# Kernel tuning notes

Hardware: AMD Instinct MI355X
Metric: run time of the kernel (lower is better)

The kernel has to match this reference:

```python
import jax, jax.numpy as jnp
import numpy as np
from jax import lax

NUM_VARS = 64
T_MAX = 2048
EMBED_DIM = 512
GRU_H = 64
FINAL_H = 64
OUT_DIM = 1


def setup_inputs() -> dict:
    key = jax.random.key(0)
    ks = jax.random.split(key, 12)
    s_e = 1.0 / np.sqrt(EMBED_DIM)
    s_h = 1.0 / np.sqrt(GRU_H)
    s_c = 1.0 / np.sqrt(NUM_VARS * GRU_H)
    s_f = 1.0 / np.sqrt(FINAL_H)
    return {
        "embeddings": jax.random.normal(ks[0], (NUM_VARS, T_MAX, EMBED_DIM), jnp.float32),
        "lengths": jax.random.randint(ks[1], (NUM_VARS,), 0, T_MAX),
        # GRU params, PyTorch layout: gate order r, z, n
        "W_ih": jax.random.uniform(ks[2], (3 * GRU_H, EMBED_DIM), jnp.float32, -s_h, s_h),
        "W_hh": jax.random.uniform(ks[3], (3 * GRU_H, GRU_H), jnp.float32, -s_h, s_h),
        "b_ih": jax.random.uniform(ks[4], (3 * GRU_H,), jnp.float32, -s_h, s_h),
        "b_hh": jax.random.uniform(ks[5], (3 * GRU_H,), jnp.float32, -s_h, s_h),
        # MLP params
        "W1": jax.random.uniform(ks[6], (FINAL_H, NUM_VARS * GRU_H), jnp.float32, -s_c, s_c),
        "b1": jax.random.uniform(ks[7], (FINAL_H,), jnp.float32, -s_c, s_c),
        "W2": jax.random.uniform(ks[8], (OUT_DIM, FINAL_H), jnp.float32, -s_f, s_f),
        "b2": jax.random.uniform(ks[9], (OUT_DIM,), jnp.float32, -s_f, s_f),
    }


def _gru_final_hidden(embeddings, lengths, W_ih, W_hh, b_ih, b_hh):
    # embeddings: [V, T, E]; shared GRU run over all variables in one batched scan.
    V, T, E = embeddings.shape
    H = W_hh.shape[1]
    # Precompute input-to-gate projections for all timesteps: [V, T, 3H] -> [T, V, 3H]
    x_gates = jnp.einsum('vte,ge->tvg', embeddings, W_ih) + b_ih

    def step(h, inp):
        xg, t = inp  # xg: [V, 3H]
        hg = h @ W_hh.T + b_hh  # [V, 3H]
        xr, xz, xn = jnp.split(xg, 3, axis=-1)
        hr, hz, hn = jnp.split(hg, 3, axis=-1)
        r = jax.nn.sigmoid(xr + hr)
        z = jax.nn.sigmoid(xz + hz)
        n = jnp.tanh(xn + r * hn)
        h_new = (1.0 - z) * n + z * h
        # freeze state past each variable's length (length 0 -> stays zeros)
        h = jnp.where((t < lengths)[:, None], h_new, h)
        return h, None

    h0 = jnp.zeros((V, H), embeddings.dtype)
    hT, _ = lax.scan(step, h0, (x_gates, jnp.arange(T)))
    return hT  # [V, H]


def reference(embeddings, lengths, W_ih, W_hh, b_ih, b_hh, W1, b1, W2, b2):
    hT = _gru_final_hidden(embeddings, lengths, W_ih, W_hh, b_ih, b_hh)
    concat = hT.reshape(-1)  # [V*H], same order as torch.cat of per-var summaries
    hid = jax.nn.relu(concat @ W1.T + b1)
    return hid @ W2.T + b2  # [out_dim]
```

## Files before the change

### kernel.cpp

```cpp
#include <hip/hip_runtime.h>
#include <math.h>

#define V 64
#define TMAX 2048
#define ED 512
#define H 64
#define G3 192

__global__ void k_init(float* __restrict__ h) {
    int i = blockIdx.x * blockDim.x + threadIdx.x;
    if (i < V * H) h[i] = 0.f;
}

__global__ __launch_bounds__(256) void k_gemm(
    const float* __restrict__ emb, const int* __restrict__ lengths,
    const float* __restrict__ W_ih, const float* __restrict__ b_ih,
    float* __restrict__ xg, int c, int CT) {
    int v   = blockIdx.y;
    int tl0 = blockIdx.x * 128;
    int t0  = c * CT + tl0;
    int len = lengths[v];
    if (t0 >= len) return;

    __shared__ __align__(16) float Es[128 * 64];
    __shared__ __align__(16) float Ws[G3 * 64];

    int th = threadIdx.x;
    int tb = th & 15;
    int gb = th >> 4;
    int eswz = tb & 7;

    float acc[8][12];
#pragma unroll
    for (int i = 0; i < 8; i++)
#pragma unroll
        for (int j = 0; j < 12; j++) acc[i][j] = 0.f;

    const float* ebase = emb + (size_t)(v * TMAX + t0) * ED;

    for (int kc = 0; kc < 8; kc++) {
#pragma unroll
        for (int r = 0; r < 8; r++) {
            int i = th + r * 256;
            int row = i >> 4, pos = i & 15;
            *(float4*)&Es[row * 64 + (pos ^ ((row >> 3) & 7)) * 4] =
                *(const float4*)&ebase[(size_t)row * ED + kc * 64 + pos * 4];
        }
#pragma unroll
        for (int r = 0; r < 12; r++) {
            int i = th + r * 256;
            int row = i >> 4, pos = i & 15;
            *(float4*)&Ws[row * 64 + (pos ^ (row & 7)) * 4] =
                *(const float4*)&W_ih[(size_t)row * ED + kc * 64 + pos * 4];
        }
        __syncthreads();
#pragma unroll 2
        for (int k4 = 0; k4 < 16; k4++) {
            float4 e[8];
#pragma unroll
            for (int i = 0; i < 8; i++)
                e[i] = *(float4*)&Es[(tb * 8 + i) * 64 + (k4 ^ eswz) * 4];
#pragma unroll
            for (int j = 0; j < 12; j++) {
                int g = gb * 12 + j;
                float4 w = *(float4*)&Ws[g * 64 + (k4 ^ (g & 7)) * 4];
#pragma unroll
                for (int i = 0; i < 8; i++)
                    acc[i][j] += e[i].x * w.x + e[i].y * w.y + e[i].z * w.z + e[i].w * w.w;
            }
        }
        __syncthreads();
    }

    float4 bv[3];
#pragma unroll
    for (int j4 = 0; j4 < 3; j4++)
        bv[j4] = *(const float4*)&b_ih[gb * 12 + j4 * 4];

#pragma unroll
    for (int i = 0; i < 8; i++) {
        size_t ob = ((size_t)(v * CT + tl0 + tb * 8 + i)) * G3 + gb * 12;
#pragma unroll
        for (int j4 = 0; j4 < 3; j4++) {
            float4 o;
            o.x = acc[i][j4 * 4 + 0] + bv[j4].x;
            o.y = acc[i][j4 * 4 + 1] + bv[j4].y;
            o.z = acc[i][j4 * 4 + 2] + bv[j4].z;
            o.w = acc[i][j4 * 4 + 3] + bv[j4].w;
            *(float4*)&xg[ob + j4 * 4] = o;
        }
    }
}

__global__ __launch_bounds__(256) void k_gemm_s(
    const float* __restrict__ emb, const int* __restrict__ lengths,
    const float* __restrict__ W_ih, const float* __restrict__ b_ih,
    float* __restrict__ xg, int c, int CT) {
    int v   = blockIdx.y;
    int tl0 = blockIdx.x * 32;
    int t0  = c * CT + tl0;
    int len = lengths[v];
    if (t0 >= len) return;

    __shared__ __align__(16) float Es[32][68];
    __shared__ __align__(16) float Ws[G3][68];

    int th = threadIdx.x;
    int tq = th & 31;
    int gq = th >> 5;

    float acc[24];
#pragma unroll
    for (int j = 0; j < 24; j++) acc[j] = 0.f;

    for (int kc = 0; kc < 8; kc++) {
#pragma unroll
        for (int r = 0; r < 2; r++) {
            int i = th + r * 256;
            int row = i >> 4, pos = i & 15;
            *(float4*)&Es[row][pos * 4] =
                *(const float4*)&emb[((size_t)(v * TMAX + t0 + row)) * ED + kc * 64 + pos * 4];
        }
#pragma unroll
        for (int r = 0; r < 12; r++) {
            int i = th + r * 256;
            int row = i >> 4, pos = i & 15;
            *(float4*)&Ws[row][pos * 4] =
                *(const float4*)&W_ih[(size_t)row * ED + kc * 64 + pos * 4];
        }
        __syncthreads();
#pragma unroll
        for (int k4 = 0; k4 < 16; k4++) {
            float4 e4 = *(float4*)&Es[tq][k4 * 4];
#pragma unroll
            for (int j = 0; j < 24; j++) {
                float4 w4 = *(float4*)&Ws[gq * 24 + j][k4 * 4];
                acc[j] += e4.x * w4.x + e4.y * w4.y + e4.z * w4.z + e4.w * w4.w;
            }
        }
        __syncthreads();
    }

    size_t ob = ((size_t)(v * CT + tl0 + tq)) * G3 + gq * 24;
#pragma unroll
    for (int j4 = 0; j4 < 6; j4++) {
        float4 o;
        o.x = acc[j4 * 4 + 0] + b_ih[gq * 24 + j4 * 4 + 0];
        o.y = acc[j4 * 4 + 1] + b_ih[gq * 24 + j4 * 4 + 1];
        o.z = acc[j4 * 4 + 2] + b_ih[gq * 24 + j4 * 4 + 2];
        o.w = acc[j4 * 4 + 3] + b_ih[gq * 24 + j4 * 4 + 3];
        *(float4*)&xg[ob + j4 * 4] = o;
    }
}

__global__ __launch_bounds__(192) void k_rec(
    const float* __restrict__ xg, const int* __restrict__ lengths,
    const float* __restrict__ W_hh, const float* __restrict__ b_hh,
    float* __restrict__ h, int c, int CT) {
    int v  = blockIdx.x;
    int th = threadIdx.x;
    int len = lengths[v];
    int rem = len - c * CT;
    int tcnt = rem < 0 ? 0 : (rem > CT ? CT : rem);

    __shared__ __align__(16) float hs[H];
    __shared__ float znbuf[128];

    float4 w4[16];
#pragma unroll
    for (int k4 = 0; k4 < 16; k4++)
        w4[k4] = *(const float4*)&W_hh[(size_t)th * H + k4 * 4];
    float bhh = b_hh[th];

    if (th < H) hs[th] = h[v * H + th];
    __syncthreads();

    const float* xgv = xg + (size_t)v * CT * G3;
    float xr = 0.f, xz = 0.f, xn = 0.f;
    if (th < H && tcnt > 0) {
        xr = xgv[th]; xz = xgv[64 + th]; xn = xgv[128 + th];
    }

    for (int t = 0; t < tcnt; t++) {
        float pr = 0.f, pz = 0.f, pn = 0.f;
        if (th < H && t + 1 < tcnt) {
            const float* p = xgv + (size_t)(t + 1) * G3;
            pr = p[th]; pz = p[64 + th]; pn = p[128 + th];
        }
        float a0 = 0.f, a1 = 0.f, a2 = 0.f, a3 = 0.f;
#pragma unroll
        for (int k4 = 0; k4 < 4; k4++) {
            float4 h4 = *(float4*)&hs[k4 * 4];
            a0 += w4[k4].x * h4.x + w4[k4].y * h4.y + w4[k4].z * h4.z + w4[k4].w * h4.w;
        }
#pragma unroll
        for (int k4 = 4; k4 < 8; k4++) {
            float4 h4 = *(float4*)&hs[k4 * 4];
            a1 += w4[k4].x * h4.x + w4[k4].y * h4.y + w4[k4].z * h4.z + w4[k4].w * h4.w;
        }
#pragma unroll
        for (int k4 = 8; k4 < 12; k4++) {
            float4 h4 = *(float4*)&hs[k4 * 4];
            a2 += w4[k4].x * h4.x + w4[k4].y * h4.y + w4[k4].z * h4.z + w4[k4].w * h4.w;
        }
#pragma unroll
        for (int k4 = 12; k4 < 16; k4++) {
            float4 h4 = *(float4*)&hs[k4 * 4];
            a3 += w4[k4].x * h4.x + w4[k4].y * h4.y + w4[k4].z * h4.z + w4[k4].w * h4.w;
        }
        float hg = bhh + ((a0 + a1) + (a2 + a3));

        if (th >= H) znbuf[th - H] = hg;
        __syncthreads();
        if (th < H) {
            float r = __fdividef(1.f, 1.f + __expf(-(hg + xr)));
            float z = __fdividef(1.f, 1.f + __expf(-(znbuf[th] + xz)));
            float pre = xn + r * znbuf[64 + th];
            float e2 = __expf(2.f * pre);
            float n = 1.f - __fdividef(2.f, e2 + 1.f);
            float hold = hs[th];
            hs[th] = (1.f - z) * n + z * hold;
            xr = pr; xz = pz; xn = pn;
        }
        __syncthreads();
    }
    if (th < H) h[v * H + th] = hs[th];
}

__global__ __launch_bounds__(192) void k_rec_fused(
    const float* __restrict__ emb, const int* __restrict__ lengths,
    const float* __restrict__ W_ih, const float* __restrict__ b_ih,
    const float* __restrict__ W_hh, const float* __restrict__ b_hh,
    float* __restrict__ h) {
    int v  = blockIdx.x;
    int th = threadIdx.x;
    int len = lengths[v];

    __shared__ __align__(16) float hs[H];
    __shared__ __align__(16) float es[ED];
    __shared__ float znbuf[128];
    __shared__ float xnbuf[64];

    float4 w4[16];
#pragma unroll
    for (int k4 = 0; k4 < 16; k4++)
        w4[k4] = *(const float4*)&W_hh[(size_t)th * H + k4 * 4];
    float bhh = b_hh[th];
    float bih = b_ih[th];
    if (th < H) hs[th] = 0.f;
    const float* ev = emb + (size_t)v * TMAX * ED;
    const float* wrow = W_ih + (size_t)th * ED;

    for (int t = 0; t < len; t++) {
        __syncthreads();
        for (int i = th; i < 128; i += 192)
            *(float4*)&es[i * 4] = *(const float4*)&ev[(size_t)t * ED + i * 4];
        __syncthreads();
        float xgt = bih;
        for (int k4 = 0; k4 < 128; k4++) {
            float4 wv = *(const float4*)&wrow[k4 * 4];
            float4 e4 = *(float4*)&es[k4 * 4];
            xgt += wv.x * e4.x + wv.y * e4.y + wv.z * e4.z + wv.w * e4.w;
        }
        float hg = bhh;
#pragma unroll
        for (int k4 = 0; k4 < 16; k4++) {
            float4 h4 = *(float4*)&hs[k4 * 4];
            hg += w4[k4].x * h4.x + w4[k4].y * h4.y + w4[k4].z * h4.z + w4[k4].w * h4.w;
        }
        if (th >= H && th < 128) znbuf[th - H] = hg + xgt;
        if (th >= 128) { znbuf[th - H] = hg; xnbuf[th - 128] = xgt; }
        __syncthreads();
        if (th < H) {
            float r = 1.f / (1.f + expf(-(hg + xgt)));
            float z = 1.f / (1.f + expf(-znbuf[th]));
            float n = tanhf(xnbuf[th] + r * znbuf[64 + th]);
            float hold = hs[th];
            hs[th] = (1.f - z) * n + z * hold;
        }
    }
    __syncthreads();
    if (th < H) h[v * H + th] = hs[th];
}

__global__ __launch_bounds__(256) void k_mlp1(
    const float* __restrict__ h, const float* __restrict__ W1,
    const float* __restrict__ b1, float* __restrict__ hid) {
    int o = blockIdx.x, th = threadIdx.x;
    const float* w = W1 + (size_t)o * (V * H);
    float s = 0.f;
#pragma unroll
    for (int r = 0; r < 4; r++) {
        int i = (th + r * 256) * 4;
        float4 a = *(const float4*)&w[i];
        float4 b = *(const float4*)&h[i];
        s += a.x * b.x + a.y * b.y + a.z * b.z + a.w * b.w;
    }
    __shared__ float red[4];
    for (int off = 32; off; off >>= 1) s += __shfl_down(s, off);
    if ((th & 63) == 0) red[th >> 6] = s;
    __syncthreads();
    if (th == 0) {
        float tot = red[0] + red[1] + red[2] + red[3] + b1[o];
        hid[o] = tot > 0.f ? tot : 0.f;
    }
}

__global__ void k_mlp2(const float* __restrict__ hid, const float* __restrict__ W2,
                       const float* __restrict__ b2, float* __restrict__ out) {
    int th = threadIdx.x;
    float s = hid[th] * W2[th];
    for (int off = 32; off; off >>= 1) s += __shfl_down(s, off);
    if (th == 0) out[0] = s + b2[0];
}

extern "C" void kernel_launch(void* const* d_in, const int* in_sizes, int n_in,
                              void* d_out, int out_size, void* d_ws, size_t ws_size,
                              hipStream_t stream) {
    const float* emb     = (const float*)d_in[0];
    const int*   lengths = (const int*)d_in[1];
    const float* W_ih    = (const float*)d_in[2];
    const float* W_hh    = (const float*)d_in[3];
    const float* b_ih    = (const float*)d_in[4];
    const float* b_hh    = (const float*)d_in[5];
    const float* W1      = (const float*)d_in[6];
    const float* b1      = (const float*)d_in[7];
    const float* W2      = (const float*)d_in[8];
    const float* b2      = (const float*)d_in[9];
    float* out = (float*)d_out;
    float* wsf = (float*)d_ws;

    const size_t tail = (size_t)V * H + V;
    int CT = 0;
    const int cts[7] = {2048, 1024, 512, 256, 128, 64, 32};
    for (int i = 0; i < 7; i++) {
        size_t need = ((size_t)V * cts[i] * G3 + tail) * sizeof(float);
        if (need <= ws_size) { CT = cts[i]; break; }
    }

    if (CT > 0) {
        float* xg  = wsf;
        float* hbf = wsf + (size_t)V * CT * G3;
        float* hid = hbf + (size_t)V * H;
        k_init<<<dim3((V * H + 255) / 256), dim3(256), 0, stream>>>(hbf);
        int nch = TMAX / CT;
        for (int c = 0; c < nch; c++) {
            if (CT >= 256)
                k_gemm<<<dim3(CT / 128, V), dim3(256), 0, stream>>>(emb, lengths, W_ih, b_ih, xg, c, CT);
            else
                k_gemm_s<<<dim3(CT / 32, V), dim3(256), 0, stream>>>(emb, lengths, W_ih, b_ih, xg, c, CT);
            k_rec<<<dim3(V), dim3(G3), 0, stream>>>(xg, lengths, W_hh, b_hh, hbf, c, CT);
        }
        k_mlp1<<<dim3(V), dim3(256), 0, stream>>>(hbf, W1, b1, hid);
        k_mlp2<<<dim3(1), dim3(64), 0, stream>>>(hid, W2, b2, out);
    } else {
        float* hbf = wsf;
        float* hid = hbf + (size_t)V * H;
        k_rec_fused<<<dim3(V), dim3(G3), 0, stream>>>(emb, lengths, W_ih, b_ih, W_hh, b_hh, hbf);
        k_mlp1<<<dim3(V), dim3(256), 0, stream>>>(hbf, W1, b1, hid);
        k_mlp2<<<dim3(1), dim3(64), 0, stream>>>(hid, W2, b2, out);
    }
}
```

Baseline: 1.841 ms.

## Run GRU recurrence with one wavefront per variable using packed FMA

Restructures the recurrent kernel from 192 threads (one per gate row) to 64 threads, where each thread holds all three gate rows of W_hh in registers and computes r, z and n itself. This removes the shared-memory exchange buffer and both __syncthreads per timestep, relying on single-wavefront lockstep to keep the hidden-state shared array consistent. The dot products use v_pk_fma_f32 inline assembly to do two FMAs per instruction. It raises register use to about 192 floats of weights per thread and depends on wave64 execution with no barrier between the write and the next read of the shared state.

```diff
diff --git a/kernel.cpp b/kernel.cpp
--- a/kernel.cpp
+++ b/kernel.cpp
@@ -6,6 +6,10 @@
 #define ED 512
 #define H 64
 #define G3 192
+
+__device__ __forceinline__ void pk_fma(float2& acc, float2 a, float2 b) {
+    asm("v_pk_fma_f32 %0, %1, %2, %0" : "+v"(acc) : "v"(a), "v"(b));
+}
 
 __global__ void k_init(float* __restrict__ h) {
     int i = blockIdx.x * blockDim.x + threadIdx.x;
@@ -153,78 +157,71 @@
     }
 }
 
-__global__ __launch_bounds__(192) void k_rec(
+__global__ __launch_bounds__(64) void k_rec(
     const float* __restrict__ xg, const int* __restrict__ lengths,
     const float* __restrict__ W_hh, const float* __restrict__ b_hh,
     float* __restrict__ h, int c, int CT) {
-    int v  = blockIdx.x;
-    int th = threadIdx.x;
+    int v = blockIdx.x;
+    int i = threadIdx.x;
     int len = lengths[v];
     int rem = len - c * CT;
     int tcnt = rem < 0 ? 0 : (rem > CT ? CT : rem);
 
     __shared__ __align__(16) float hs[H];
-    __shared__ float znbuf[128];
-
-    float4 w4[16];
-#pragma unroll
-    for (int k4 = 0; k4 < 16; k4++)
-        w4[k4] = *(const float4*)&W_hh[(size_t)th * H + k4 * 4];
-    float bhh = b_hh[th];
-
-    if (th < H) hs[th] = h[v * H + th];
-    __syncthreads();
+
+    float2 wr[32], wz[32], wn[32];
+    {
+        const float2* Wr = (const float2*)&W_hh[(size_t)i * H];
+        const float2* Wz = (const float2*)&W_hh[(size_t)(64 + i) * H];
+        const float2* Wn = (const float2*)&W_hh[(size_t)(128 + i) * H];
+#pragma unroll
+        for (int k = 0; k < 32; k++) { wr[k] = Wr[k]; wz[k] = Wz[k]; wn[k] = Wn[k]; }
+    }
+    float br = b_hh[i], bz = b_hh[64 + i], bn = b_hh[128 + i];
+
+    float hown = h[v * H + i];
+    hs[i] = hown;
 
     const float* xgv = xg + (size_t)v * CT * G3;
     float xr = 0.f, xz = 0.f, xn = 0.f;
-    if (th < H && tcnt > 0) {
-        xr = xgv[th]; xz = xgv[64 + th]; xn = xgv[128 + th];
-    }
+    if (tcnt > 0) { xr = xgv[i]; xz = xgv[64 + i]; xn = xgv[128 + i]; }
 
     for (int t = 0; t < tcnt; t++) {
         float pr = 0.f, pz = 0.f, pn = 0.f;
-        if (th < H && t + 1 < tcnt) {
+        if (t + 1 < tcnt) {
             const float* p = xgv + (size_t)(t + 1) * G3;
-            pr = p[th]; pz = p[64 + th]; pn = p[128 + th];
-        }
-        float a0 = 0.f, a1 = 0.f, a2 = 0.f, a3 = 0.f;
-#pragma unroll
-        for (int k4 = 0; k4 < 4; k4++) {
-            float4 h4 = *(float4*)&hs[k4 * 4];
-            a0 += w4[k4].x * h4.x + w4[k4].y * h4.y + w4[k4].z * h4.z + w4[k4].w * h4.w;
-        }
-#pragma unroll
-        for (int k4 = 4; k4 < 8; k4++) {
-            float4 h4 = *(float4*)&hs[k4 * 4];
-            a1 += w4[k4].x * h4.x + w4[k4].y * h4.y + w4[k4].z * h4.z + w4[k4].w * h4.w;
-        }
-#pragma unroll
-        for (int k4 = 8; k4 < 12; k4++) {
-            float4 h4 = *(float4*)&hs[k4 * 4];
-            a2 += w4[k4].x * h4.x + w4[k4].y * h4.y + w4[k4].z * h4.z + w4[k4].w * h4.w;
-        }
-#pragma unroll
-        for (int k4 = 12; k4 < 16; k4++) {
-            float4 h4 = *(float4*)&hs[k4 * 4];
-            a3 += w4[k4].x * h4.x + w4[k4].y * h4.y + w4[k4].z * h4.z + w4[k4].w * h4.w;
-        }
-        float hg = bhh + ((a0 + a1) + (a2 + a3));
-
-        if (th >= H) znbuf[th - H] = hg;
-        __syncthreads();
-        if (th < H) {
-            float r = __fdividef(1.f, 1.f + __expf(-(hg + xr)));
-            float z = __fdividef(1.f, 1.f + __expf(-(znbuf[th] + xz)));
-            float pre = xn + r * znbuf[64 + th];
-            float e2 = __expf(2.f * pre);
-            float n = 1.f - __fdividef(2.f, e2 + 1.f);
-            float hold = hs[th];
-            hs[th] = (1.f - z) * n + z * hold;
-            xr = pr; xz = pz; xn = pn;
-        }
-        __syncthreads();
-    }
-    if (th < H) h[v * H + th] = hs[th];
+            pr = p[i]; pz = p[64 + i]; pn = p[128 + i];
+        }
+        float2 ar0 = {0.f,0.f}, ar1 = {0.f,0.f};
+        float2 az0 = {0.f,0.f}, az1 = {0.f,0.f};
+        float2 an0 = {0.f,0.f}, an1 = {0.f,0.f};
+#pragma unroll
+        for (int q = 0; q < 16; q++) {
+            float4 h4 = *(const float4*)&hs[q * 4];
+            float2 hlo = make_float2(h4.x, h4.y);
+            float2 hhi = make_float2(h4.z, h4.w);
+            pk_fma(ar0, wr[2 * q],     hlo);
+            pk_fma(ar1, wr[2 * q + 1], hhi);
+            pk_fma(az0, wz[2 * q],     hlo);
+            pk_fma(az1, wz[2 * q + 1], hhi);
+            pk_fma(an0, wn[2 * q],     hlo);
+            pk_fma(an1, wn[2 * q + 1], hhi);
+        }
+        float hr = br + ((ar0.x + ar0.y) + (ar1.x + ar1.y));
+        float hz = bz + ((az0.x + az0.y) + (az1.x + az1.y));
+        float hn = bn + ((an0.x + an0.y) + (an1.x + an1.y));
+
+        float r = __fdividef(1.f, 1.f + __expf(-(hr + xr)));
+        float z = __fdividef(1.f, 1.f + __expf(-(hz + xz)));
+        float pre = xn + r * hn;
+        float e2 = __expf(2.f * pre);
+        float n = 1.f - __fdividef(2.f, e2 + 1.f);
+        hown = (1.f - z) * n + z * hown;
+
+        hs[i] = hown;
+        xr = pr; xz = pz; xn = pn;
+    }
+    if (tcnt > 0) h[v * H + i] = hown;
 }
 
 __global__ __launch_bounds__(192) void k_rec_fused(
@@ -349,7 +346,7 @@
                 k_gemm<<<dim3(CT / 128, V), dim3(256), 0, stream>>>(emb, lengths, W_ih, b_ih, xg, c, CT);
             else
                 k_gemm_s<<<dim3(CT / 32, V), dim3(256), 0, stream>>>(emb, lengths, W_ih, b_ih, xg, c, CT);
-            k_rec<<<dim3(V), dim3(G3), 0, stream>>>(xg, lengths, W_hh, b_hh, hbf, c, CT);
+            k_rec<<<dim3(V), dim3(64), 0, stream>>>(xg, lengths, W_hh, b_hh, hbf, c, CT);
         }
         k_mlp1<<<dim3(V), dim3(256), 0, stream>>>(hbf, W1, b1, hid);
         k_mlp2<<<dim3(1), dim3(64), 0, stream>>>(hid, W2, b2, out);
```

After: 2.165 ms. 1.18x slower.

## Restructure GRU recurrence to split gate nonlinearities across warps with packed FMA

Applied to the files above, without the earlier changes.

The recurrent kernel now has each of the three 64-thread groups compute its own gate activation: the r and z groups apply sigmoid and publish it to shared memory, and the n group finishes the update. This replaces the previous scheme where one group did all the nonlinear work serially. The inner dot products use v_pk_fma_f32 packed FMAs, and the loop is unrolled by four timesteps with xg prefetched a group ahead (indices clamped and masked by tcnt). Waves-per-EU attributes are also set on both kernels. The change aims to shorten the per-step serial critical path, at the cost of inline asm and a fixed occupancy hint.

```diff
diff --git a/kernel.cpp b/kernel.cpp
--- a/kernel.cpp
+++ b/kernel.cpp
@@ -7,12 +7,17 @@
 #define H 64
 #define G3 192
 
+__device__ __forceinline__ void pk_fma(float2& acc, float2 a, float2 b) {
+    asm("v_pk_fma_f32 %0, %1, %2, %0" : "+v"(acc) : "v"(a), "v"(b));
+}
+
 __global__ void k_init(float* __restrict__ h) {
     int i = blockIdx.x * blockDim.x + threadIdx.x;
     if (i < V * H) h[i] = 0.f;
 }
 
-__global__ __launch_bounds__(256) void k_gemm(
+__global__ __launch_bounds__(256)
+__attribute__((amdgpu_waves_per_eu(2, 2))) void k_gemm(
     const float* __restrict__ emb, const int* __restrict__ lengths,
     const float* __restrict__ W_ih, const float* __restrict__ b_ih,
     float* __restrict__ xg, int c, int CT) {
@@ -153,78 +158,97 @@
     }
 }
 
-__global__ __launch_bounds__(192) void k_rec(
+#define LD4(DST, T0)                                                        \
+  {                                                                         \
+    int u0 = (T0)     < tcnt ? (T0)     : tcnt - 1;                         \
+    int u1 = (T0) + 1 < tcnt ? (T0) + 1 : tcnt - 1;                         \
+    int u2 = (T0) + 2 < tcnt ? (T0) + 2 : tcnt - 1;                         \
+    int u3 = (T0) + 3 < tcnt ? (T0) + 3 : tcnt - 1;                         \
+    DST.x = xgt[(size_t)u0 * G3];                                           \
+    DST.y = xgt[(size_t)u1 * G3];                                           \
+    DST.z = xgt[(size_t)u2 * G3];                                           \
+    DST.w = xgt[(size_t)u3 * G3];                                           \
+  }
+
+#define STEP(XV, TT)                                                        \
+  {                                                                         \
+    float2 a0 = {0.f, 0.f}, a1 = {0.f, 0.f}, a2 = {0.f, 0.f},               \
+           a3 = {0.f, 0.f};                                                 \
+    _Pragma("unroll")                                                       \
+    for (int k4 = 0; k4 < 16; k4 += 2) {                                    \
+      float4 ha = *(const float4*)&hs[k4 * 4];                              \
+      float4 hb = *(const float4*)&hs[k4 * 4 + 4];                          \
+      pk_fma(a0, make_float2(w4[k4].x, w4[k4].y), make_float2(ha.x, ha.y)); \
+      pk_fma(a1, make_float2(w4[k4].z, w4[k4].w), make_float2(ha.z, ha.w)); \
+      pk_fma(a2, make_float2(w4[k4+1].x, w4[k4+1].y),                       \
+                 make_float2(hb.x, hb.y));                                  \
+      pk_fma(a3, make_float2(w4[k4+1].z, w4[k4+1].w),                       \
+                 make_float2(hb.z, hb.w));                                  \
+    }                                                                       \
+    float hg = bhh + ((a0.x + a0.y) + (a1.x + a1.y)) +                      \
+                     ((a2.x + a2.y) + (a3.x + a3.y));                       \
+    if (gate == 0) {                                                        \
+      rz[o] = __fdividef(1.f, 1.f + __expf(-(hg + (XV))));                  \
+    } else if (gate == 1) {                                                 \
+      rz[64 + o] = __fdividef(1.f, 1.f + __expf(-(hg + (XV))));             \
+    }                                                                       \
+    __syncthreads();                                                        \
+    if (gate == 2) {                                                        \
+      float rv = rz[o], zv = rz[64 + o];                                    \
+      float e2 = __expf(2.f * ((XV) + rv * hg));                            \
+      float nv = 1.f - __fdividef(2.f, e2 + 1.f);                           \
+      float hnew = (1.f - zv) * nv + zv * hprev;                            \
+      hprev = ((TT) < tcnt) ? hnew : hprev;                                 \
+      hs[o] = hprev;                                                        \
+    }                                                                       \
+    __syncthreads();                                                        \
+  }
+
+__global__ __attribute__((amdgpu_flat_work_group_size(192, 192),
+                          amdgpu_waves_per_eu(1, 1))) void k_rec(
     const float* __restrict__ xg, const int* __restrict__ lengths,
     const float* __restrict__ W_hh, const float* __restrict__ b_hh,
     float* __restrict__ h, int c, int CT) {
-    int v  = blockIdx.x;
-    int th = threadIdx.x;
-    int len = lengths[v];
-    int rem = len - c * CT;
+    int v    = blockIdx.x;
+    int th   = threadIdx.x;
+    int o    = th & 63;
+    int gate = th >> 6;
+    int len  = lengths[v];
+    int rem  = len - c * CT;
     int tcnt = rem < 0 ? 0 : (rem > CT ? CT : rem);
 
     __shared__ __align__(16) float hs[H];
-    __shared__ float znbuf[128];
+    __shared__ float rz[128];
 
     float4 w4[16];
 #pragma unroll
     for (int k4 = 0; k4 < 16; k4++)
         w4[k4] = *(const float4*)&W_hh[(size_t)th * H + k4 * 4];
+#pragma unroll
+    for (int k4 = 0; k4 < 16; k4++)
+        asm volatile("" : "+v"(w4[k4].x), "+v"(w4[k4].y),
+                          "+v"(w4[k4].z), "+v"(w4[k4].w));
     float bhh = b_hh[th];
 
-    if (th < H) hs[th] = h[v * H + th];
+    float hprev = h[v * H + o];
+    if (th < H) hs[th] = hprev;
     __syncthreads();
 
-    const float* xgv = xg + (size_t)v * CT * G3;
-    float xr = 0.f, xz = 0.f, xn = 0.f;
-    if (th < H && tcnt > 0) {
-        xr = xgv[th]; xz = xgv[64 + th]; xn = xgv[128 + th];
-    }
-
-    for (int t = 0; t < tcnt; t++) {
-        float pr = 0.f, pz = 0.f, pn = 0.f;
-        if (th < H && t + 1 < tcnt) {
-            const float* p = xgv + (size_t)(t + 1) * G3;
-            pr = p[th]; pz = p[64 + th]; pn = p[128 + th];
-        }
-        float a0 = 0.f, a1 = 0.f, a2 = 0.f, a3 = 0.f;
-#pragma unroll
-        for (int k4 = 0; k4 < 4; k4++) {
-            float4 h4 = *(float4*)&hs[k4 * 4];
-            a0 += w4[k4].x * h4.x + w4[k4].y * h4.y + w4[k4].z * h4.z + w4[k4].w * h4.w;
-        }
-#pragma unroll
-        for (int k4 = 4; k4 < 8; k4++) {
-            float4 h4 = *(float4*)&hs[k4 * 4];
-            a1 += w4[k4].x * h4.x + w4[k4].y * h4.y + w4[k4].z * h4.z + w4[k4].w * h4.w;
-        }
-#pragma unroll
-        for (int k4 = 8; k4 < 12; k4++) {
-            float4 h4 = *(float4*)&hs[k4 * 4];
-            a2 += w4[k4].x * h4.x + w4[k4].y * h4.y + w4[k4].z * h4.z + w4[k4].w * h4.w;
-        }
-#pragma unroll
-        for (int k4 = 12; k4 < 16; k4++) {
-            float4 h4 = *(float4*)&hs[k4 * 4];
-            a3 += w4[k4].x * h4.x + w4[k4].y * h4.y + w4[k4].z * h4.z + w4[k4].w * h4.w;
-        }
-        float hg = bhh + ((a0 + a1) + (a2 + a3));
-
-        if (th >= H) znbuf[th - H] = hg;
-        __syncthreads();
-        if (th < H) {
-            float r = __fdividef(1.f, 1.f + __expf(-(hg + xr)));
-            float z = __fdividef(1.f, 1.f + __expf(-(znbuf[th] + xz)));
-            float pre = xn + r * znbuf[64 + th];
-            float e2 = __expf(2.f * pre);
-            float n = 1.f - __fdividef(2.f, e2 + 1.f);
-            float hold = hs[th];
-            hs[th] = (1.f - z) * n + z * hold;
-            xr = pr; xz = pz; xn = pn;
-        }
-        __syncthreads();
-    }
-    if (th < H) h[v * H + th] = hs[th];
+    const float* xgt = xg + (size_t)v * CT * G3 + th;
+
+    if (tcnt > 0) {
+        float4 xc, xp;
+        LD4(xc, 0);
+        for (int t0 = 0; t0 < tcnt; t0 += 4) {
+            LD4(xp, t0 + 4);
+            STEP(xc.x, t0 + 0);
+            STEP(xc.y, t0 + 1);
+            STEP(xc.z, t0 + 2);
+            STEP(xc.w, t0 + 3);
+            xc = xp;
+        }
+        if (gate == 2) h[v * H + o] = hprev;
+    }
 }
 
 __global__ __launch_bounds__(192) void k_rec_fused(
```

New measurement: 1.613 ms. -12.4%, faster.
